# Kernel tuning notes

Hardware: AMD Instinct MI355X
Metric: run time of the kernel (lower is better)

The kernel has to match this reference:

```python
import jax, jax.numpy as jnp
import numpy as np

EPS = 1e-5  # torch BatchNorm1d default eps


def _bn_train(h, gamma, beta):
    # BatchNorm1d in training mode over the edge (batch) axes: biased variance.
    m = jnp.mean(h, axis=(0, 1), keepdims=True)
    v = jnp.mean(jnp.square(h - m), axis=(0, 1), keepdims=True)
    return (h - m) * jax.lax.rsqrt(v + EPS) * gamma + beta


def setup_inputs() -> dict:
    key = jax.random.key(0)
    ks = jax.random.split(key, 12)
    N, F, H = 1024, 128, 128
    s1 = 1.0 / np.sqrt(2 * F)
    s2 = 1.0 / np.sqrt(H)
    return {
        "x": jax.random.normal(ks[0], (N, F), dtype=jnp.float32),
        "W1": jax.random.uniform(ks[1], (H, 2 * F), jnp.float32, -s1, s1),
        "b1": jax.random.uniform(ks[2], (H,), jnp.float32, -s1, s1),
        "W2": jax.random.uniform(ks[3], (H, H), jnp.float32, -s2, s2),
        "b2": jax.random.uniform(ks[4], (H,), jnp.float32, -s2, s2),
        "W3": jax.random.uniform(ks[5], (1, H), jnp.float32, -s2, s2),
        "b3": jax.random.uniform(ks[6], (1,), jnp.float32, -s2, s2),
        "g1": jnp.ones((H,), jnp.float32),
        "be1": jnp.zeros((H,), jnp.float32),
        "g2": jnp.ones((H,), jnp.float32),
        "be2": jnp.zeros((H,), jnp.float32),
    }


def reference(x, W1, b1, W2, b2, W3, b3, g1, be1, g2, be2):
    N, F = x.shape
    # Edge e = i*N + j pairs [x[j], x[i]] (row=j varies fast, col=i slow).
    # First Linear on the concat splits into two low-rank GEMMs + broadcast add,
    # avoiding the [N^2, 2F] materialization (same math as Linear(concat)).
    Wa, Wb = W1[:, :F], W1[:, F:]
    A = x @ Wa.T            # contribution of x[row] = x[j] -> varies over axis 1
    B = x @ Wb.T            # contribution of x[col] = x[i] -> varies over axis 0
    h = A[None, :, :] + B[:, None, :] + b1      # [N, N, H], h[i, j]
    h = jax.nn.relu(_bn_train(h, g1, be1))
    h = jnp.einsum('ijh,kh->ijk', h, W2) + b2   # [N, N, H]
    h = jax.nn.relu(_bn_train(h, g2, be2))
    logits = jnp.einsum('ijh,kh->ijk', h, W3)[..., 0] + b3[0]  # [N, N]
    adj = jax.nn.sigmoid((logits + logits.T) * 0.5)
    adj = adj - jnp.diag(jnp.diag(adj))
    return adj
```

## Files before the change

kernel.cpp:

```cpp
#include <hip/hip_runtime.h>
#include <hip/hip_bf16.h>

typedef _Float16 f16x8 __attribute__((ext_vector_type(8)));
typedef _Float16 f16x4 __attribute__((ext_vector_type(4)));
typedef float    f32x4 __attribute__((ext_vector_type(4)));

#define EPSV 1e-5f

__global__ __launch_bounds__(256) void k_ab(const float* __restrict__ x,
                                            const float* __restrict__ W1,
                                            const float* __restrict__ W2,
                                            _Float16* __restrict__ Apf,
                                            _Float16* __restrict__ Btf,
                                            float* __restrict__ gs,
                                            unsigned int* __restrict__ w2p) {
  __shared__ float xs[4 * 128];
  int t = threadIdx.x;
  if (blockIdx.x >= 256) {
    int c = (blockIdx.x - 256) * 256 + t;
    int pair = c & 3;
    int col  = (c >> 2) & 15;
    int quad = (c >> 6) & 3;
    int nt   = (c >> 8) & 7;
    int ks   = (c >> 11) & 3;
    int k = nt * 16 + col;
    int hch = ks * 32 + quad * 8 + pair * 2;
    _Float16 b0 = (_Float16)W2[k * 128 + hch];
    _Float16 b1 = (_Float16)W2[k * 128 + hch + 1];
    unsigned int u0 = *(unsigned short*)&b0, u1 = *(unsigned short*)&b1;
    w2p[c] = u0 | (u1 << 16);
    return;
  }
  int j0 = blockIdx.x * 4;
  for (int idx = t; idx < 512; idx += 256) xs[idx] = x[j0 * 128 + idx];
  __syncthreads();
  int h = t & 127, half = t >> 7;
  const float4* wrow = (const float4*)(W1 + h * 256 + half * 128);
  const float4* xs4 = (const float4*)xs;
  float a0 = 0.f, a1 = 0.f, a2 = 0.f, a3 = 0.f;
#pragma unroll 8
  for (int ch = 0; ch < 32; ++ch) {
    float4 wv = wrow[ch];
    float4 x0 = xs4[ch], x1 = xs4[32 + ch], x2 = xs4[64 + ch], x3 = xs4[96 + ch];
    a0 += wv.x * x0.x + wv.y * x0.y + wv.z * x0.z + wv.w * x0.w;
    a1 += wv.x * x1.x + wv.y * x1.y + wv.z * x1.z + wv.w * x1.w;
    a2 += wv.x * x2.x + wv.y * x2.y + wv.z * x2.z + wv.w * x2.w;
    a3 += wv.x * x3.x + wv.y * x3.y + wv.z * x3.z + wv.w * x3.w;
  }
  if (half == 0) {
    int S = j0 >> 7, s = (j0 >> 4) & 7, colb = j0 & 15;
    int ks = h >> 5, quad = (h >> 3) & 3, eh = (h >> 2) & 1, pos = h & 3;
    int base = S * 16384 + ((s * 4 + ks) * 64 + quad * 16 + colb) * 8 + eh * 4 + pos;
    Apf[base]      = (_Float16)a0;
    Apf[base + 8]  = (_Float16)a1;
    Apf[base + 16] = (_Float16)a2;
    Apf[base + 24] = (_Float16)a3;
  } else {
    Btf[(j0 + 0) * 128 + h] = (_Float16)a0;
    Btf[(j0 + 1) * 128 + h] = (_Float16)a1;
    Btf[(j0 + 2) * 128 + h] = (_Float16)a2;
    Btf[(j0 + 3) * 128 + h] = (_Float16)a3;
  }
  float s = a0 + a1 + a2 + a3;
  float q = a0 * a0 + a1 * a1 + a2 * a2 + a3 * a3;
  atomicAdd(&gs[half * 256 + h], s);
  atomicAdd(&gs[half * 256 + 128 + h], q);
}

__device__ __forceinline__ void f16x8_to_f32(f16x8 v, f32x4& lo, f32x4& hi) {
  f16x4 l4 = __builtin_shufflevector(v, v, 0, 1, 2, 3);
  f16x4 h4 = __builtin_shufflevector(v, v, 4, 5, 6, 7);
  lo = __builtin_convertvector(l4, f32x4);
  hi = __builtin_convertvector(h4, f32x4);
}
__device__ __forceinline__ f16x8 f32_to_f16x8(f32x4 lo, f32x4 hi) {
  f16x4 l4 = __builtin_convertvector(lo, f16x4);
  f16x4 h4 = __builtin_convertvector(hi, f16x4);
  return __builtin_shufflevector(l4, h4, 0, 1, 2, 3, 4, 5, 6, 7);
}

template <int PASS>
__global__ __launch_bounds__(256) void k_pass(
    const _Float16* __restrict__ Apf, const _Float16* __restrict__ Btf,
    const unsigned int* __restrict__ w2p,
    const float* __restrict__ gs, const float* __restrict__ g1,
    const float* __restrict__ be1,
    float* __restrict__ sum2, const float* __restrict__ g2,
    const float* __restrict__ be2, const float* __restrict__ W3v,
    const float* __restrict__ b3p, float* __restrict__ L) {
  __shared__ unsigned int ats[8192];
  __shared__ float red[1024];
  __shared__ unsigned int btl[512];
  __shared__ float P[2048];
  int t = threadIdx.x;
  int bid = blockIdx.x;
  int bj = bid & 7, bi = bid >> 3;
  int lane = t & 63, w = t >> 6;
  int ig = w >> 1, kg = w & 1;
  int col = lane & 15, quad = lane >> 4;

  const unsigned int* atsrc = (const unsigned int*)Apf + bj * 8192;
#pragma unroll
  for (int it = 0; it < 8; ++it) {
    int g = w * 8 + it;
    __builtin_amdgcn_global_load_lds(
        (const __attribute__((address_space(1))) unsigned int*)(atsrc + g * 256 + lane * 4),
        (__attribute__((address_space(3))) unsigned int*)(ats + g * 256),
        16, 0, 0);
  }

  if (t < 128) {
    const float inv = 1.f / 1024.f;
    float mA = gs[t] * inv;
    float vA = gs[128 + t] * inv - mA * mA;
    float mB = gs[256 + t] * inv;
    float vB = gs[384 + t] * inv - mB * mB;
    float sc = g1[t] * rsqrtf(vA + vB + EPSV);
    red[t] = sc;
    red[128 + t] = be1[t] - mA * sc;
    red[256 + t] = -mB * sc;
  }

  f16x8 bw[4][4];
#pragma unroll
  for (int ks = 0; ks < 4; ++ks)
#pragma unroll
    for (int nt = 0; nt < 4; ++nt)
      bw[ks][nt] = *(const f16x8*)((const _Float16*)w2p +
                                   (((ks * 8 + kg * 4 + nt) * 64) + lane) * 8);

  float al[4], uu[4], w3l[4];
  float b3v = 0.f;
  if (PASS == 2) {
    b3v = b3p[0];
    const float invM = 1.f / (1024.f * 1024.f);
#pragma unroll
    for (int nt = 0; nt < 4; ++nt) {
      int k = (kg * 4 + nt) * 16 + col;
      float mdot = sum2[k] * invM;
      float var = sum2[128 + k] * invM - mdot * mdot;
      float alv = g2[k] * rsqrtf(var + EPSV);
      al[nt] = alv;
      uu[nt] = be2[k] - mdot * alv;
      w3l[nt] = W3v[k];
    }
  }
  __syncthreads();

  {
    int h0 = ((t >> 6) & 3) * 32 + ((t >> 4) & 3) * 8;
    f32x4 scl = *(const f32x4*)(red + h0);
    f32x4 sch = *(const f32x4*)(red + h0 + 4);
    f32x4 tal = *(const f32x4*)(red + 128 + h0);
    f32x4 tah = *(const f32x4*)(red + 128 + h0 + 4);
#pragma unroll
    for (int k = 0; k < 8; ++k) {
      unsigned int* p = ats + t * 4 + k * 1024;
      f16x8 v = *(f16x8*)p;
      f32x4 lo, hi;
      f16x8_to_f32(v, lo, hi);
      lo = lo * scl + tal;
      hi = hi * sch + tah;
      *(f16x8*)p = f32_to_f16x8(lo, hi);
    }
  }

  if (t < 128) {
    int r = t >> 4, c8 = (t & 15) * 8;
    f16x8 braw = *(const f16x8*)(Btf + (bi * 8 + r) * 128 + c8);
    f32x4 lo, hi;
    f16x8_to_f32(braw, lo, hi);
    f32x4 sl = *(const f32x4*)(red + c8);
    f32x4 sh = *(const f32x4*)(red + c8 + 4);
    f32x4 tl = *(const f32x4*)(red + 256 + c8);
    f32x4 th = *(const f32x4*)(red + 256 + c8 + 4);
    lo = lo * sl + tl;
    hi = hi * sh + th;
    *(f16x8*)((_Float16*)btl + r * 128 + c8) = f32_to_f16x8(lo, hi);
  }
  __syncthreads();

  float s1[4], s2[4];
  if (PASS == 1) {
#pragma unroll
    for (int nt = 0; nt < 4; ++nt) { s1[nt] = 0.f; s2[nt] = 0.f; }
  }

  const f16x8 zz = {(_Float16)0, (_Float16)0, (_Float16)0, (_Float16)0,
                    (_Float16)0, (_Float16)0, (_Float16)0, (_Float16)0};

  for (int il = 0; il < 4; ++il) {
    f16x8 btr[4];
#pragma unroll
    for (int ks = 0; ks < 4; ++ks)
      btr[ks] = *(const f16x8*)((const _Float16*)btl + (ig * 4 + il) * 128 + ks * 32 + quad * 8);

    for (int s = 0; s < 8; ++s) {
      f32x4 acc[4];
#pragma unroll
      for (int nt = 0; nt < 4; ++nt) acc[nt] = (f32x4){0.f, 0.f, 0.f, 0.f};

#pragma unroll
      for (int ks = 0; ks < 4; ++ks) {
        f16x8 af = *(const f16x8*)(ats + ((s * 4 + ks) * 64 + lane) * 4);
        f16x8 a = __builtin_elementwise_max(af + btr[ks], zz);
#pragma unroll
        for (int nt = 0; nt < 4; ++nt)
          acc[nt] = __builtin_amdgcn_mfma_f32_16x16x32_f16(a, bw[ks][nt], acc[nt], 0, 0, 0);
      }

      if (PASS == 1) {
#pragma unroll
        for (int nt = 0; nt < 4; ++nt)
#pragma unroll
          for (int r = 0; r < 4; ++r) {
            float d = acc[nt][r];
            s1[nt] += d;
            s2[nt] = fmaf(d, d, s2[nt]);
          }
      } else {
        float rsum[4] = {0.f, 0.f, 0.f, 0.f};
#pragma unroll
        for (int nt = 0; nt < 4; ++nt)
#pragma unroll
          for (int r = 0; r < 4; ++r) {
            float h = fmaxf(fmaf(acc[nt][r], al[nt], uu[nt]), 0.f);
            rsum[r] = fmaf(h, w3l[nt], rsum[r]);
          }
#pragma unroll
        for (int r = 0; r < 4; ++r) {
          rsum[r] += __shfl_xor(rsum[r], 1);
          rsum[r] += __shfl_xor(rsum[r], 2);
          rsum[r] += __shfl_xor(rsum[r], 4);
          rsum[r] += __shfl_xor(rsum[r], 8);
        }
        if (col == 0) {
          int slot = kg * 1024 + (ig * 4 + il) * 128 + s * 16 + quad * 4;
#pragma unroll
          for (int r = 0; r < 4; ++r) P[slot + r] = rsum[r];
        }
      }
    }
  }

  if (PASS == 1) {
#pragma unroll
    for (int nt = 0; nt < 4; ++nt) {
      s1[nt] += __shfl_xor(s1[nt], 16);
      s1[nt] += __shfl_xor(s1[nt], 32);
      s2[nt] += __shfl_xor(s2[nt], 16);
      s2[nt] += __shfl_xor(s2[nt], 32);
    }
    __syncthreads();
    if (lane < 16) {
#pragma unroll
      for (int nt = 0; nt < 4; ++nt) {
        red[w * 128 + nt * 16 + lane] = s1[nt];
        red[w * 128 + 64 + nt * 16 + lane] = s2[nt];
      }
    }
    __syncthreads();
    {
      int k = t & 127;
      int kgc = k >> 6;
      int loc = k & 63;
      int off = (t >> 7) * 64;
      float v = red[kgc * 128 + off + loc] + red[(2 + kgc) * 128 + off + loc];
      atomicAdd(&sum2[(t >> 7) * 128 + k], v);
    }
  } else {
    __syncthreads();
#pragma unroll
    for (int rep = 0; rep < 4; ++rep) {
      int slot = rep * 256 + t;
      float v = P[slot] + P[1024 + slot] + b3v;
      int i = bi * 8 + (slot >> 7);
      int j = bj * 128 + (slot & 127);
      L[i * 1024 + j] = v;
    }
  }
}

__global__ __launch_bounds__(256) void k_adj(const float* __restrict__ L,
                                             float* __restrict__ out) {
  __shared__ float ldsT[64 * 65];
  int t = threadIdx.x;
  int ti = blockIdx.x >> 4, tj = blockIdx.x & 15;
  int r = t >> 2, fq = t & 3;

  const float* srow = L + (tj * 64 + r) * 1024 + ti * 64;
#pragma unroll
  for (int e = 0; e < 4; ++e) {
    int c0 = (e * 4 + fq) * 4;
    float4 v = *(const float4*)(srow + c0);
    ldsT[r * 65 + c0 + 0] = v.x;
    ldsT[r * 65 + c0 + 1] = v.y;
    ldsT[r * 65 + c0 + 2] = v.z;
    ldsT[r * 65 + c0 + 3] = v.w;
  }
  __syncthreads();

  int gi = ti * 64 + r;
  const float* arow = L + gi * 1024 + tj * 64;
#pragma unroll
  for (int e = 0; e < 4; ++e) {
    int c0 = (e * 4 + fq) * 4;
    float4 a = *(const float4*)(arow + c0);
    float b0 = ldsT[(c0 + 0) * 65 + r];
    float b1 = ldsT[(c0 + 1) * 65 + r];
    float b2 = ldsT[(c0 + 2) * 65 + r];
    float b3 = ldsT[(c0 + 3) * 65 + r];
    float4 o;
    o.x = 1.f / (1.f + __expf(-0.5f * (a.x + b0)));
    o.y = 1.f / (1.f + __expf(-0.5f * (a.y + b1)));
    o.z = 1.f / (1.f + __expf(-0.5f * (a.z + b2)));
    o.w = 1.f / (1.f + __expf(-0.5f * (a.w + b3)));
    if (ti == tj) {
      int j0 = tj * 64 + c0;
      if (gi == j0) o.x = 0.f;
      if (gi == j0 + 1) o.y = 0.f;
      if (gi == j0 + 2) o.z = 0.f;
      if (gi == j0 + 3) o.w = 0.f;
    }
    *(float4*)(out + gi * 1024 + tj * 64 + c0) = o;
  }
}

extern "C" void kernel_launch(void* const* d_in, const int* in_sizes, int n_in,
                              void* d_out, int out_size, void* d_ws, size_t ws_size,
                              hipStream_t stream) {
  const float* x   = (const float*)d_in[0];
  const float* W1  = (const float*)d_in[1];
  const float* W2  = (const float*)d_in[3];
  const float* W3  = (const float*)d_in[5];
  const float* b3  = (const float*)d_in[6];
  const float* g1  = (const float*)d_in[7];
  const float* be1 = (const float*)d_in[8];
  const float* g2  = (const float*)d_in[9];
  const float* be2 = (const float*)d_in[10];

  float* ws = (float*)d_ws;
  _Float16* Apf     = (_Float16*)ws;
  _Float16* Btf     = (_Float16*)(ws + 65536);
  unsigned int* w2p = (unsigned int*)(ws + 131072);
  float* gs         = ws + 139264;
  float* sum2       = ws + 139776;
  float* L          = ws + 140032;
  float* out        = (float*)d_out;


  k_ab<<<288, 256, 0, stream>>>(x, W1, W2, Apf, Btf, gs, w2p);
  k_pass<1><<<1024, 256, 0, stream>>>(Apf, Btf, w2p, gs, g1, be1, sum2,
                                      nullptr, nullptr, nullptr, nullptr, nullptr);
  k_pass<2><<<1024, 256, 0, stream>>>(Apf, Btf, w2p, gs, g1, be1, sum2,
                                      g2, be2, W3, b3, L);
  k_adj<<<256, 256, 0, stream>>>(L, out);
}
```

Baseline: 191.3 us.

## Double rows per block and write partial logits directly, summing halves in adjacency kernel

Each k_pass block now covers 16 rows of i instead of 8, halving the grid to 512 blocks so each block's A tile loaded into LDS and its weight registers serve twice as many rows. The LDS staging buffer P and its final reduction are removed. The two k-group partial logits are written straight to two global arrays L0/L1, and k_adj adds them and applies b3. This cuts per-block setup and LDS use but adds an extra 4MB write and read of partial logits, and fewer blocks may reduce occupancy or load balance.

Measured after the change: 190.6 us. No clear change (-0.4%).

```diff
diff --git a/kernel.cpp b/kernel.cpp
--- a/kernel.cpp
+++ b/kernel.cpp
@@ -87,11 +87,10 @@
     const float* __restrict__ be1,
     float* __restrict__ sum2, const float* __restrict__ g2,
     const float* __restrict__ be2, const float* __restrict__ W3v,
-    const float* __restrict__ b3p, float* __restrict__ L) {
+    float* __restrict__ L0, float* __restrict__ L1) {
   __shared__ unsigned int ats[8192];
   __shared__ float red[1024];
-  __shared__ unsigned int btl[512];
-  __shared__ float P[2048];
+  __shared__ unsigned int btl[1024];
   int t = threadIdx.x;
   int bid = blockIdx.x;
   int bj = bid & 7, bi = bid >> 3;
@@ -130,9 +129,7 @@
                                    (((ks * 8 + kg * 4 + nt) * 64) + lane) * 8);
 
   float al[4], uu[4], w3l[4];
-  float b3v = 0.f;
   if (PASS == 2) {
-    b3v = b3p[0];
     const float invM = 1.f / (1024.f * 1024.f);
 #pragma unroll
     for (int nt = 0; nt < 4; ++nt) {
@@ -165,9 +162,9 @@
     }
   }
 
-  if (t < 128) {
+  {
     int r = t >> 4, c8 = (t & 15) * 8;
-    f16x8 braw = *(const f16x8*)(Btf + (bi * 8 + r) * 128 + c8);
+    f16x8 braw = *(const f16x8*)(Btf + (bi * 16 + r) * 128 + c8);
     f32x4 lo, hi;
     f16x8_to_f32(braw, lo, hi);
     f32x4 sl = *(const f32x4*)(red + c8);
@@ -189,11 +186,11 @@
   const f16x8 zz = {(_Float16)0, (_Float16)0, (_Float16)0, (_Float16)0,
                     (_Float16)0, (_Float16)0, (_Float16)0, (_Float16)0};
 
-  for (int il = 0; il < 4; ++il) {
+  for (int il = 0; il < 8; ++il) {
     f16x8 btr[4];
 #pragma unroll
     for (int ks = 0; ks < 4; ++ks)
-      btr[ks] = *(const f16x8*)((const _Float16*)btl + (ig * 4 + il) * 128 + ks * 32 + quad * 8);
+      btr[ks] = *(const f16x8*)((const _Float16*)btl + (ig * 8 + il) * 128 + ks * 32 + quad * 8);
 
     for (int s = 0; s < 8; ++s) {
       f32x4 acc[4];
@@ -235,9 +232,10 @@
           rsum[r] += __shfl_xor(rsum[r], 8);
         }
         if (col == 0) {
-          int slot = kg * 1024 + (ig * 4 + il) * 128 + s * 16 + quad * 4;
-#pragma unroll
-          for (int r = 0; r < 4; ++r) P[slot + r] = rsum[r];
+          int i = bi * 16 + ig * 8 + il;
+          float* Lk = kg ? L1 : L0;
+          float4 v = make_float4(rsum[0], rsum[1], rsum[2], rsum[3]);
+          *(float4*)(&Lk[i * 1024 + bj * 128 + s * 16 + quad * 4]) = v;
         }
       }
     }
@@ -268,53 +266,52 @@
       float v = red[kgc * 128 + off + loc] + red[(2 + kgc) * 128 + off + loc];
       atomicAdd(&sum2[(t >> 7) * 128 + k], v);
     }
-  } else {
-    __syncthreads();
-#pragma unroll
-    for (int rep = 0; rep < 4; ++rep) {
-      int slot = rep * 256 + t;
-      float v = P[slot] + P[1024 + slot] + b3v;
-      int i = bi * 8 + (slot >> 7);
-      int j = bj * 128 + (slot & 127);
-      L[i * 1024 + j] = v;
-    }
-  }
-}
-
-__global__ __launch_bounds__(256) void k_adj(const float* __restrict__ L,
+  }
+}
+
+__global__ __launch_bounds__(256) void k_adj(const float* __restrict__ L0,
+                                             const float* __restrict__ L1,
+                                             const float* __restrict__ b3p,
                                              float* __restrict__ out) {
   __shared__ float ldsT[64 * 65];
   int t = threadIdx.x;
+  float b3v = b3p[0];
   int ti = blockIdx.x >> 4, tj = blockIdx.x & 15;
   int r = t >> 2, fq = t & 3;
 
-  const float* srow = L + (tj * 64 + r) * 1024 + ti * 64;
+  {
+    const float* s0 = L0 + (tj * 64 + r) * 1024 + ti * 64;
+    const float* s1 = L1 + (tj * 64 + r) * 1024 + ti * 64;
+#pragma unroll
+    for (int e = 0; e < 4; ++e) {
+      int c0 = (e * 4 + fq) * 4;
+      float4 v0 = *(const float4*)(s0 + c0);
+      float4 v1 = *(const float4*)(s1 + c0);
+      ldsT[r * 65 + c0 + 0] = v0.x + v1.x;
+      ldsT[r * 65 + c0 + 1] = v0.y + v1.y;
+      ldsT[r * 65 + c0 + 2] = v0.z + v1.z;
+      ldsT[r * 65 + c0 + 3] = v0.w + v1.w;
+    }
+  }
+  __syncthreads();
+
+  int gi = ti * 64 + r;
+  const float* a0r = L0 + gi * 1024 + tj * 64;
+  const float* a1r = L1 + gi * 1024 + tj * 64;
 #pragma unroll
   for (int e = 0; e < 4; ++e) {
     int c0 = (e * 4 + fq) * 4;
-    float4 v = *(const float4*)(srow + c0);
-    ldsT[r * 65 + c0 + 0] = v.x;
-    ldsT[r * 65 + c0 + 1] = v.y;
-    ldsT[r * 65 + c0 + 2] = v.z;
-    ldsT[r * 65 + c0 + 3] = v.w;
-  }
-  __syncthreads();
-
-  int gi = ti * 64 + r;
-  const float* arow = L + gi * 1024 + tj * 64;
-#pragma unroll
-  for (int e = 0; e < 4; ++e) {
-    int c0 = (e * 4 + fq) * 4;
-    float4 a = *(const float4*)(arow + c0);
+    float4 a0 = *(const float4*)(a0r + c0);
+    float4 a1 = *(const float4*)(a1r + c0);
     float b0 = ldsT[(c0 + 0) * 65 + r];
     float b1 = ldsT[(c0 + 1) * 65 + r];
     float b2 = ldsT[(c0 + 2) * 65 + r];
     float b3 = ldsT[(c0 + 3) * 65 + r];
     float4 o;
-    o.x = 1.f / (1.f + __expf(-0.5f * (a.x + b0)));
-    o.y = 1.f / (1.f + __expf(-0.5f * (a.y + b1)));
-    o.z = 1.f / (1.f + __expf(-0.5f * (a.z + b2)));
-    o.w = 1.f / (1.f + __expf(-0.5f * (a.w + b3)));
+    o.x = 1.f / (1.f + __expf(-(0.5f * (a0.x + a1.x + b0) + b3v)));
+    o.y = 1.f / (1.f + __expf(-(0.5f * (a0.y + a1.y + b1) + b3v)));
+    o.z = 1.f / (1.f + __expf(-(0.5f * (a0.z + a1.z + b2) + b3v)));
+    o.w = 1.f / (1.f + __expf(-(0.5f * (a0.w + a1.w + b3) + b3v)));
     if (ti == tj) {
       int j0 = tj * 64 + c0;
       if (gi == j0) o.x = 0.f;
@@ -345,14 +342,15 @@
   unsigned int* w2p = (unsigned int*)(ws + 131072);
   float* gs         = ws + 139264;
   float* sum2       = ws + 139776;
-  float* L          = ws + 140032;
+  float* L0         = ws + 140032;
+  float* L1         = ws + 1188608;
   float* out        = (float*)d_out;
 
 
   k_ab<<<288, 256, 0, stream>>>(x, W1, W2, Apf, Btf, gs, w2p);
-  k_pass<1><<<1024, 256, 0, stream>>>(Apf, Btf, w2p, gs, g1, be1, sum2,
-                                      nullptr, nullptr, nullptr, nullptr, nullptr);
-  k_pass<2><<<1024, 256, 0, stream>>>(Apf, Btf, w2p, gs, g1, be1, sum2,
-                                      g2, be2, W3, b3, L);
-  k_adj<<<256, 256, 0, stream>>>(L, out);
-}
+  k_pass<1><<<512, 256, 0, stream>>>(Apf, Btf, w2p, gs, g1, be1, sum2,
+                                     nullptr, nullptr, nullptr, nullptr, nullptr);
+  k_pass<2><<<512, 256, 0, stream>>>(Apf, Btf, w2p, gs, g1, be1, sum2,
+                                     g2, be2, W3, L0, L1);
+  k_adj<<<256, 256, 0, stream>>>(L0, L1, b3, out);
+}
```
